# Optimization experiments

Measured on AMD Instinct MI355X. Metric: run time of the kernel, lower is better.

Reference implementation:

```python
import jax, jax.numpy as jnp
import numpy as np

N = 50000      # nodes
E = 400000     # edges (before self loops)
IN = 256       # in_channels
HID = 128      # hidden_channels
HEADS = 4
OUT = 256      # out_channels
NEG = 0.2      # LeakyReLU negative slope (PyG default)


def _glorot(key, shape, fan_in):
    return jax.random.normal(key, shape, jnp.float32) * (1.0 / np.sqrt(fan_in))


def setup_inputs() -> dict:
    key = jax.random.key(0)
    ks = jax.random.split(key, 8)
    x = jax.random.normal(ks[0], (N, IN), jnp.float32)
    edge_index = jax.random.randint(ks[1], (2, E), 0, N, dtype=jnp.int64)
    # layer 1: GATv2Conv(IN -> HID, heads=HEADS, concat=True)
    W1l = _glorot(ks[2], (IN, HEADS * HID), IN)           # source transform
    W1r = _glorot(ks[3], (IN, HEADS * HID), IN)           # target transform
    a1 = _glorot(ks[4], (HEADS, HID), HID)                # attention vector per head
    b1 = jnp.zeros((HEADS * HID,), jnp.float32)
    # layer 2: GATv2Conv(HEADS*HID -> OUT, heads=1, concat=False)
    W2l = _glorot(ks[5], (HEADS * HID, OUT), HEADS * HID)
    W2r = _glorot(ks[6], (HEADS * HID, OUT), HEADS * HID)
    a2 = _glorot(ks[7], (1, OUT), OUT)
    b2 = jnp.zeros((OUT,), jnp.float32)
    return dict(x=x, edge_index=edge_index, W1l=W1l, W1r=W1r, a1=a1, b1=b1,
                W2l=W2l, W2r=W2r, a2=a2, b2=b2)


def gatv2_conv(x, src, dst, Wl, Wr, att, bias, heads, ch, concat):
    """PyG GATv2Conv (add_self_loops already applied to src/dst).
    message j->i uses x_l[j]; score = att . leaky_relu(x_l[j] + x_r[i])."""
    n = x.shape[0]
    xl = (x @ Wl).reshape(n, heads, ch)   # [N,H,C] source features
    xr = (x @ Wr).reshape(n, heads, ch)   # [N,H,C] target features
    g = xl[src] + xr[dst]                 # [E',H,C] gathered per edge
    e = jnp.einsum('ehc,hc->eh', jax.nn.leaky_relu(g, NEG), att)  # [E',H]
    # segment softmax over incoming edges of each dst node
    e_max = jax.ops.segment_max(e, dst, num_segments=n)
    p = jnp.exp(e - e_max[dst])
    denom = jax.ops.segment_sum(p, dst, num_segments=n)
    alpha = p / denom[dst]                # [E',H]
    out = jax.ops.segment_sum(alpha[:, :, None] * xl[src], dst, num_segments=n)
    out = out.reshape(n, heads * ch) if concat else out.mean(axis=1)
    return out + bias


def reference(x, edge_index, W1l, W1r, a1, b1, W2l, W2r, a2, b2):
    loop = jnp.arange(x.shape[0], dtype=edge_index.dtype)
    src = jnp.concatenate([edge_index[0], loop])  # add self loops (PyG default)
    dst = jnp.concatenate([edge_index[1], loop])
    h = jax.nn.relu(gatv2_conv(x, src, dst, W1l, W1r, a1, b1, HEADS, HID, True))
    return gatv2_conv(h, src, dst, W2l, W2r, a2, b2, 1, OUT, False)
```

## Files before the change

kernel.cpp:

```cpp
#include <hip/hip_runtime.h>
#include <cstdint>
#include <cstddef>

#define NNODES 50000
#define NEDGES 400000
#define INC    256
#define D1     512
#define OUTC   256
#define NEG    0.2f
#define NB     196

typedef __attribute__((ext_vector_type(8))) short short8;
typedef __attribute__((ext_vector_type(4))) short bf16x4;
typedef __attribute__((ext_vector_type(4))) float f32x4;

__device__ inline short f2bf(float f) {
  union { float f; uint32_t u; } v; v.f = f;
  uint32_t r = (v.u + 0x7fffu + ((v.u >> 16) & 1u)) >> 16;
  return (short)(r & 0xffffu);
}
__device__ inline float bf2f(short s) {
  union { uint32_t u; float f; } v;
  v.u = ((uint32_t)(uint16_t)s) << 16;
  return v.f;
}

__global__ __launch_bounds__(256) void cvt_x_k(const float* __restrict__ x,
                                               short* __restrict__ xb) {
  size_t base = ((size_t)blockIdx.x * 256 + threadIdx.x) * 8;
  f32x4 a = *(const f32x4*)&x[base];
  f32x4 b = *(const f32x4*)&x[base + 4];
  short8 o;
  o[0] = f2bf(a[0]); o[1] = f2bf(a[1]); o[2] = f2bf(a[2]); o[3] = f2bf(a[3]);
  o[4] = f2bf(b[0]); o[5] = f2bf(b[1]); o[6] = f2bf(b[2]); o[7] = f2bf(b[3]);
  *(short8*)&xb[base] = o;
}

__global__ __launch_bounds__(256) void twb_k(const float* __restrict__ W,
                                             short* __restrict__ WT,
                                             int K, int N) {
  __shared__ float tile[32][33];
  int tx = threadIdx.x & 31, ty = threadIdx.x >> 5;
  int n0 = blockIdx.x * 32, k0 = blockIdx.y * 32;
#pragma unroll
  for (int i = 0; i < 4; ++i)
    tile[ty + i * 8][tx] = W[(size_t)(k0 + ty + i * 8) * N + n0 + tx];
  __syncthreads();
#pragma unroll
  for (int i = 0; i < 4; ++i) {
    int n = ty + i * 8;
    WT[(size_t)(n0 + n) * K + k0 + tx] = f2bf(tile[tx][n]);
  }
}

#define LDT 72
template<bool BF16OUT>
__global__ __launch_bounds__(256) void gemm_bf16_k(const short* __restrict__ A,
    const short* __restrict__ BT, void* __restrict__ Cv, int M, int K, int Nc) {
  __shared__ short As[128 * LDT];
  __shared__ short Bs[128 * LDT];
  const int tid = threadIdx.x;
  const int lane = tid & 63, wave = tid >> 6;
  const int wr = wave >> 1, wc = wave & 1;
  const int l15 = lane & 15, l4 = lane >> 4;
  const int bm = blockIdx.y * 128, bn = blockIdx.x * 128;

  f32x4 zero4 = {0.f, 0.f, 0.f, 0.f};
  f32x4 acc[4][4];
#pragma unroll
  for (int m = 0; m < 4; ++m)
#pragma unroll
    for (int n = 0; n < 4; ++n) acc[m][n] = zero4;

  for (int k0 = 0; k0 < K; k0 += 64) {
#pragma unroll
    for (int i = 0; i < 4; ++i) {
      int q = tid + 256 * i;
      int row = q >> 3, kc = q & 7;
      short8 va = {0, 0, 0, 0, 0, 0, 0, 0};
      int gr = bm + row;
      if (gr < M) va = *(const short8*)&A[(size_t)gr * K + k0 + kc * 8];
      *(short8*)&As[row * LDT + kc * 8] = va;
      short8 vb = *(const short8*)&BT[(size_t)(bn + row) * K + k0 + kc * 8];
      *(short8*)&Bs[row * LDT + kc * 8] = vb;
    }
    __syncthreads();
    short8 af[4][2], bf[4][2];
#pragma unroll
    for (int m = 0; m < 4; ++m)
#pragma unroll
      for (int kk = 0; kk < 2; ++kk)
        af[m][kk] = *(const short8*)&As[(wr * 64 + m * 16 + l15) * LDT + kk * 32 + l4 * 8];
#pragma unroll
    for (int n = 0; n < 4; ++n)
#pragma unroll
      for (int kk = 0; kk < 2; ++kk)
        bf[n][kk] = *(const short8*)&Bs[(wc * 64 + n * 16 + l15) * LDT + kk * 32 + l4 * 8];
#pragma unroll
    for (int kk = 0; kk < 2; ++kk)
#pragma unroll
      for (int m = 0; m < 4; ++m)
#pragma unroll
        for (int n = 0; n < 4; ++n)
          acc[m][n] = __builtin_amdgcn_mfma_f32_16x16x32_bf16(
              af[m][kk], bf[n][kk], acc[m][n], 0, 0, 0);
    __syncthreads();
  }
#pragma unroll
  for (int m = 0; m < 4; ++m) {
    int row0 = bm + wr * 64 + m * 16 + l4 * 4;
#pragma unroll
    for (int r = 0; r < 4; ++r) {
      int row = row0 + r;
      if (row < M) {
#pragma unroll
        for (int n = 0; n < 4; ++n) {
          size_t idx = (size_t)row * Nc + bn + wc * 64 + n * 16 + l15;
          if (BF16OUT) ((short*)Cv)[idx] = f2bf(acc[m][n][r]);
          else         ((float*)Cv)[idx] = acc[m][n][r];
        }
      }
    }
  }
}

__global__ __launch_bounds__(256) void zero_i_k(int* __restrict__ p, int n) {
  int stride = gridDim.x * 256;
  for (int i = blockIdx.x * 256 + threadIdx.x; i < n; i += stride) p[i] = 0;
}

__global__ __launch_bounds__(256) void hist_k(const int* __restrict__ dsts,
                                              int* __restrict__ deg) {
  int e = blockIdx.x * 256 + threadIdx.x;
  if (e < NEDGES) atomicAdd(&deg[dsts[e]], 1);
}

__global__ __launch_bounds__(256) void bsum_k(const int* __restrict__ deg,
                                              int* __restrict__ bsum) {
  __shared__ int red[256];
  int t = threadIdx.x, i = blockIdx.x * 256 + t;
  red[t] = (i < NNODES) ? deg[i] : 0;
  __syncthreads();
#pragma unroll
  for (int off = 128; off > 0; off >>= 1) {
    if (t < off) red[t] += red[t + off];
    __syncthreads();
  }
  if (t == 0) bsum[blockIdx.x] = red[0];
}

__global__ __launch_bounds__(64) void bscan_k(const int* __restrict__ bsum,
                                              int* __restrict__ bscan) {
  if (threadIdx.x == 0) {
    int run = 0;
    for (int j = 0; j < NB; ++j) { bscan[j] = run; run += bsum[j]; }
  }
}

__global__ __launch_bounds__(256) void rowptr_k(const int* __restrict__ deg,
    const int* __restrict__ bscan, int* __restrict__ rowptr,
    int* __restrict__ cursor) {
  __shared__ int s[256];
  int t = threadIdx.x, b = blockIdx.x, i = b * 256 + t;
  int v = (i < NNODES) ? deg[i] : 0;
  s[t] = v;
  __syncthreads();
#pragma unroll
  for (int off = 1; off < 256; off <<= 1) {
    int y = (t >= off) ? s[t - off] : 0;
    __syncthreads();
    s[t] += y;
    __syncthreads();
  }
  if (i < NNODES) {
    int ex = bscan[b] + s[t] - v;
    rowptr[i] = ex;
    cursor[i] = ex;
  }
  if (b == 0 && t == 0) rowptr[NNODES] = NEDGES;
}

__global__ __launch_bounds__(256) void scatter_k(const int* __restrict__ srcs,
    const int* __restrict__ dsts, int* __restrict__ cursor,
    int* __restrict__ col) {
  int e = blockIdx.x * 256 + threadIdx.x;
  if (e < NEDGES) {
    int pos = atomicAdd(&cursor[dsts[e]], 1);
    col[pos] = srcs[e];
  }
}

__global__ __launch_bounds__(256) void fused1_k(const int* __restrict__ rowptr,
    const int* __restrict__ col, const short* __restrict__ XLb,
    const float* __restrict__ XR, const float* __restrict__ a1,
    const float* __restrict__ b1, short* __restrict__ Hb) {
  int d = blockIdx.x * 4 + (threadIdx.x >> 6);
  if (d >= NNODES) return;
  int lane = threadIdx.x & 63;
  int c0 = lane * 8;
  float av[8], xr[8], acc[8];
#pragma unroll
  for (int t = 0; t < 8; ++t) {
    av[t] = a1[c0 + t];
    xr[t] = XR[(size_t)d * D1 + c0 + t];
    acc[t] = 0.f;
  }
  float den = 0.f;
  int beg = rowptr[d], end = rowptr[d + 1];
  for (int i = beg - 1; i < end; ++i) {
    int s = (i < beg) ? d : col[i];
    short8 v = *(const short8*)&XLb[(size_t)s * D1 + c0];
    float xl[8];
#pragma unroll
    for (int t = 0; t < 8; ++t) xl[t] = bf2f(v[t]);
    float part = 0.f;
#pragma unroll
    for (int t = 0; t < 8; ++t) {
      float g = xl[t] + xr[t];
      g = g > 0.f ? g : NEG * g;
      part = fmaf(g, av[t], part);
    }
    part += __shfl_xor(part, 1);
    part += __shfl_xor(part, 2);
    part += __shfl_xor(part, 4);
    part += __shfl_xor(part, 8);
    float p = __expf(part);
    den += p;
#pragma unroll
    for (int t = 0; t < 8; ++t) acc[t] = fmaf(p, xl[t], acc[t]);
  }
  short8 o;
#pragma unroll
  for (int t = 0; t < 8; ++t) {
    float hv = acc[t] / den + b1[c0 + t];
    hv = hv > 0.f ? hv : 0.f;
    o[t] = f2bf(hv);
  }
  *(short8*)&Hb[(size_t)d * D1 + c0] = o;
}

__global__ __launch_bounds__(256) void fused2_k(const int* __restrict__ rowptr,
    const int* __restrict__ col, const short* __restrict__ XLb,
    const float* __restrict__ XR, const float* __restrict__ a2,
    const float* __restrict__ b2, float* __restrict__ out) {
  int d = blockIdx.x * 4 + (threadIdx.x >> 6);
  if (d >= NNODES) return;
  int lane = threadIdx.x & 63;
  int c0 = lane * 4;
  float av[4], xr[4], acc[4];
#pragma unroll
  for (int t = 0; t < 4; ++t) {
    av[t] = a2[c0 + t];
    xr[t] = XR[(size_t)d * OUTC + c0 + t];
    acc[t] = 0.f;
  }
  float den = 0.f;
  int beg = rowptr[d], end = rowptr[d + 1];
  for (int i = beg - 1; i < end; ++i) {
    int s = (i < beg) ? d : col[i];
    bf16x4 v = *(const bf16x4*)&XLb[(size_t)s * OUTC + c0];
    float xl[4];
#pragma unroll
    for (int t = 0; t < 4; ++t) xl[t] = bf2f(v[t]);
    float part = 0.f;
#pragma unroll
    for (int t = 0; t < 4; ++t) {
      float g = xl[t] + xr[t];
      g = g > 0.f ? g : NEG * g;
      part = fmaf(g, av[t], part);
    }
#pragma unroll
    for (int off = 1; off < 64; off <<= 1) part += __shfl_xor(part, off);
    float p = __expf(part);
    den += p;
#pragma unroll
    for (int t = 0; t < 4; ++t) acc[t] = fmaf(p, xl[t], acc[t]);
  }
  f32x4 o;
#pragma unroll
  for (int t = 0; t < 4; ++t) o[t] = acc[t] / den + b2[c0 + t];
  *(f32x4*)&out[(size_t)d * OUTC + c0] = o;
}

extern "C" void kernel_launch(void* const* d_in, const int* in_sizes, int n_in,
                              void* d_out, int out_size, void* d_ws, size_t ws_size,
                              hipStream_t stream) {
  const float* x   = (const float*)d_in[0];
  const int*   ei  = (const int*)d_in[1];
  const float* W1l = (const float*)d_in[2];
  const float* W1r = (const float*)d_in[3];
  const float* a1  = (const float*)d_in[4];
  const float* b1  = (const float*)d_in[5];
  const float* W2l = (const float*)d_in[6];
  const float* W2r = (const float*)d_in[7];
  const float* a2  = (const float*)d_in[8];
  const float* b2  = (const float*)d_in[9];
  float* out = (float*)d_out;
  char* ws = (char*)d_ws;

  short* XL1b  = (short*)(ws + 0);
  float* XR1   = (float*)(ws + 51200000);
  short* XL2b  = (short*)(ws + 0);
  float* XR2   = (float*)(ws + 25600000);
  short* WT1l  = (short*)(ws + 153600000);
  short* WT1r  = (short*)(ws + 153862144);
  short* WT2l  = (short*)(ws + 154124288);
  short* WT2r  = (short*)(ws + 154386432);
  int* rowptr  = (int*)(ws + 154648576);
  int* cursor  = (int*)(ws + 154848640);
  int* colv    = (int*)(ws + 155048640);
  int* deg     = (int*)(ws + 156648640);
  int* bsum    = (int*)(ws + 156848640);
  int* bscan   = (int*)(ws + 156849536);
  short* XB = (short*)d_out;
  short* Hb = (short*)d_out;

  const int* srcs = ei;
  const int* dsts = ei + NEDGES;

  dim3 blk(256);
  int eblk = (NEDGES + 255) / 256;
  int nblk4 = (NNODES + 3) / 4;

  zero_i_k<<<64, blk, 0, stream>>>(deg, NNODES);
  hist_k<<<eblk, blk, 0, stream>>>(dsts, deg);
  bsum_k<<<NB, blk, 0, stream>>>(deg, bsum);
  bscan_k<<<1, 64, 0, stream>>>(bsum, bscan);
  rowptr_k<<<NB, blk, 0, stream>>>(deg, bscan, rowptr, cursor);
  scatter_k<<<eblk, blk, 0, stream>>>(srcs, dsts, cursor, colv);

  cvt_x_k<<<(NNODES * INC) / 2048, blk, 0, stream>>>(x, XB);
  twb_k<<<dim3(D1 / 32, INC / 32), blk, 0, stream>>>(W1l, WT1l, INC, D1);
  twb_k<<<dim3(D1 / 32, INC / 32), blk, 0, stream>>>(W1r, WT1r, INC, D1);
  twb_k<<<dim3(OUTC / 32, D1 / 32), blk, 0, stream>>>(W2l, WT2l, D1, OUTC);
  twb_k<<<dim3(OUTC / 32, D1 / 32), blk, 0, stream>>>(W2r, WT2r, D1, OUTC);

  dim3 g1(D1 / 128, (NNODES + 127) / 128);
  gemm_bf16_k<true ><<<g1, blk, 0, stream>>>(XB, WT1l, XL1b, NNODES, INC, D1);
  gemm_bf16_k<false><<<g1, blk, 0, stream>>>(XB, WT1r, XR1, NNODES, INC, D1);

  fused1_k<<<nblk4, blk, 0, stream>>>(rowptr, colv, XL1b, XR1, a1, b1, Hb);

  dim3 g2(OUTC / 128, (NNODES + 127) / 128);
  gemm_bf16_k<true ><<<g2, blk, 0, stream>>>(Hb, WT2l, XL2b, NNODES, D1, OUTC);
  gemm_bf16_k<false><<<g2, blk, 0, stream>>>(Hb, WT2r, XR2, NNODES, D1, OUTC);

  fused2_k<<<nblk4, blk, 0, stream>>>(rowptr, colv, XL2b, XR2, a2, b2, out);
}
```

Before: 494.4 us.

## Fuse left/right projections into one bf16 GEMM and unroll edge loop by two

The separate Wl and Wr weight transposes are concatenated so each layer runs a single GEMM producing an interleaved [N, 2*D] bf16 buffer. This replaces the fp32 XR output with bf16, halving that write and the later read. The aggregation kernels read xl and xr from the shared row, handle the self loop outside the main loop, and process two edges per iteration to overlap gathers and shuffle reductions. The change also stores xr at lower precision, which adds some rounding error, and widens the gathered row stride.

```diff
diff --git a/kernel.cpp b/kernel.cpp
--- a/kernel.cpp
+++ b/kernel.cpp
@@ -54,9 +54,8 @@
 }
 
 #define LDT 72
-template<bool BF16OUT>
 __global__ __launch_bounds__(256) void gemm_bf16_k(const short* __restrict__ A,
-    const short* __restrict__ BT, void* __restrict__ Cv, int M, int K, int Nc) {
+    const short* __restrict__ BT, short* __restrict__ C, int M, int K, int Nc) {
   __shared__ short As[128 * LDT];
   __shared__ short Bs[128 * LDT];
   const int tid = threadIdx.x;
@@ -114,11 +113,8 @@
       int row = row0 + r;
       if (row < M) {
 #pragma unroll
-        for (int n = 0; n < 4; ++n) {
-          size_t idx = (size_t)row * Nc + bn + wc * 64 + n * 16 + l15;
-          if (BF16OUT) ((short*)Cv)[idx] = f2bf(acc[m][n][r]);
-          else         ((float*)Cv)[idx] = acc[m][n][r];
-        }
+        for (int n = 0; n < 4; ++n)
+          C[(size_t)row * Nc + bn + wc * 64 + n * 16 + l15] = f2bf(acc[m][n][r]);
       }
     }
   }
@@ -191,82 +187,164 @@
 }
 
 __global__ __launch_bounds__(256) void fused1_k(const int* __restrict__ rowptr,
-    const int* __restrict__ col, const short* __restrict__ XLb,
-    const float* __restrict__ XR, const float* __restrict__ a1,
-    const float* __restrict__ b1, short* __restrict__ Hb) {
+    const int* __restrict__ col, const short* __restrict__ X1b,
+    const float* __restrict__ a1, const float* __restrict__ b1,
+    short* __restrict__ Hb) {
   int d = blockIdx.x * 4 + (threadIdx.x >> 6);
   if (d >= NNODES) return;
   int lane = threadIdx.x & 63;
   int c0 = lane * 8;
+  const size_t drow = (size_t)d * 1024;
   float av[8], xr[8], acc[8];
+  short8 vself = *(const short8*)&X1b[drow + c0];
+  short8 vxr   = *(const short8*)&X1b[drow + 512 + c0];
 #pragma unroll
   for (int t = 0; t < 8; ++t) {
     av[t] = a1[c0 + t];
-    xr[t] = XR[(size_t)d * D1 + c0 + t];
+    xr[t] = bf2f(vxr[t]);
     acc[t] = 0.f;
   }
   float den = 0.f;
-  int beg = rowptr[d], end = rowptr[d + 1];
-  for (int i = beg - 1; i < end; ++i) {
-    int s = (i < beg) ? d : col[i];
-    short8 v = *(const short8*)&XLb[(size_t)s * D1 + c0];
-    float xl[8];
-#pragma unroll
-    for (int t = 0; t < 8; ++t) xl[t] = bf2f(v[t]);
-    float part = 0.f;
+  {
+    float xl[8], part = 0.f;
 #pragma unroll
     for (int t = 0; t < 8; ++t) {
+      xl[t] = bf2f(vself[t]);
       float g = xl[t] + xr[t];
-      g = g > 0.f ? g : NEG * g;
+      g = fmaxf(g, NEG * g);
       part = fmaf(g, av[t], part);
     }
-    part += __shfl_xor(part, 1);
-    part += __shfl_xor(part, 2);
-    part += __shfl_xor(part, 4);
-    part += __shfl_xor(part, 8);
+    part += __shfl_xor(part, 1); part += __shfl_xor(part, 2);
+    part += __shfl_xor(part, 4); part += __shfl_xor(part, 8);
     float p = __expf(part);
     den += p;
 #pragma unroll
     for (int t = 0; t < 8; ++t) acc[t] = fmaf(p, xl[t], acc[t]);
   }
+  int beg = rowptr[d], end = rowptr[d + 1];
+  int i = beg;
+  for (; i + 1 < end; i += 2) {
+    int s0 = col[i], s1 = col[i + 1];
+    short8 v0 = *(const short8*)&X1b[(size_t)s0 * 1024 + c0];
+    short8 v1 = *(const short8*)&X1b[(size_t)s1 * 1024 + c0];
+    float xl0[8], xl1[8], p0 = 0.f, p1 = 0.f;
+#pragma unroll
+    for (int t = 0; t < 8; ++t) {
+      xl0[t] = bf2f(v0[t]);
+      float g0 = xl0[t] + xr[t]; g0 = fmaxf(g0, NEG * g0); p0 = fmaf(g0, av[t], p0);
+      xl1[t] = bf2f(v1[t]);
+      float g1 = xl1[t] + xr[t]; g1 = fmaxf(g1, NEG * g1); p1 = fmaf(g1, av[t], p1);
+    }
+    p0 += __shfl_xor(p0, 1); p1 += __shfl_xor(p1, 1);
+    p0 += __shfl_xor(p0, 2); p1 += __shfl_xor(p1, 2);
+    p0 += __shfl_xor(p0, 4); p1 += __shfl_xor(p1, 4);
+    p0 += __shfl_xor(p0, 8); p1 += __shfl_xor(p1, 8);
+    float e0 = __expf(p0), e1 = __expf(p1);
+    den += e0 + e1;
+#pragma unroll
+    for (int t = 0; t < 8; ++t) {
+      acc[t] = fmaf(e0, xl0[t], acc[t]);
+      acc[t] = fmaf(e1, xl1[t], acc[t]);
+    }
+  }
+  if (i < end) {
+    int s = col[i];
+    short8 v = *(const short8*)&X1b[(size_t)s * 1024 + c0];
+    float xl[8], part = 0.f;
+#pragma unroll
+    for (int t = 0; t < 8; ++t) {
+      xl[t] = bf2f(v[t]);
+      float g = xl[t] + xr[t];
+      g = fmaxf(g, NEG * g);
+      part = fmaf(g, av[t], part);
+    }
+    part += __shfl_xor(part, 1); part += __shfl_xor(part, 2);
+    part += __shfl_xor(part, 4); part += __shfl_xor(part, 8);
+    float p = __expf(part);
+    den += p;
+#pragma unroll
+    for (int t = 0; t < 8; ++t) acc[t] = fmaf(p, xl[t], acc[t]);
+  }
   short8 o;
 #pragma unroll
   for (int t = 0; t < 8; ++t) {
     float hv = acc[t] / den + b1[c0 + t];
-    hv = hv > 0.f ? hv : 0.f;
-    o[t] = f2bf(hv);
+    o[t] = f2bf(fmaxf(hv, 0.f));
   }
   *(short8*)&Hb[(size_t)d * D1 + c0] = o;
 }
 
 __global__ __launch_bounds__(256) void fused2_k(const int* __restrict__ rowptr,
-    const int* __restrict__ col, const short* __restrict__ XLb,
-    const float* __restrict__ XR, const float* __restrict__ a2,
-    const float* __restrict__ b2, float* __restrict__ out) {
+    const int* __restrict__ col, const short* __restrict__ X2b,
+    const float* __restrict__ a2, const float* __restrict__ b2,
+    float* __restrict__ out) {
   int d = blockIdx.x * 4 + (threadIdx.x >> 6);
   if (d >= NNODES) return;
   int lane = threadIdx.x & 63;
   int c0 = lane * 4;
+  const size_t drow = (size_t)d * 512;
   float av[4], xr[4], acc[4];
+  bf16x4 vself = *(const bf16x4*)&X2b[drow + c0];
+  bf16x4 vxr   = *(const bf16x4*)&X2b[drow + 256 + c0];
 #pragma unroll
   for (int t = 0; t < 4; ++t) {
     av[t] = a2[c0 + t];
-    xr[t] = XR[(size_t)d * OUTC + c0 + t];
+    xr[t] = bf2f(vxr[t]);
     acc[t] = 0.f;
   }
   float den = 0.f;
+  {
+    float xl[4], part = 0.f;
+#pragma unroll
+    for (int t = 0; t < 4; ++t) {
+      xl[t] = bf2f(vself[t]);
+      float g = xl[t] + xr[t];
+      g = fmaxf(g, NEG * g);
+      part = fmaf(g, av[t], part);
+    }
+#pragma unroll
+    for (int off = 1; off < 64; off <<= 1) part += __shfl_xor(part, off);
+    float p = __expf(part);
+    den += p;
+#pragma unroll
+    for (int t = 0; t < 4; ++t) acc[t] = fmaf(p, xl[t], acc[t]);
+  }
   int beg = rowptr[d], end = rowptr[d + 1];
-  for (int i = beg - 1; i < end; ++i) {
-    int s = (i < beg) ? d : col[i];
-    bf16x4 v = *(const bf16x4*)&XLb[(size_t)s * OUTC + c0];
-    float xl[4];
-#pragma unroll
-    for (int t = 0; t < 4; ++t) xl[t] = bf2f(v[t]);
-    float part = 0.f;
+  int i = beg;
+  for (; i + 1 < end; i += 2) {
+    int s0 = col[i], s1 = col[i + 1];
+    bf16x4 v0 = *(const bf16x4*)&X2b[(size_t)s0 * 512 + c0];
+    bf16x4 v1 = *(const bf16x4*)&X2b[(size_t)s1 * 512 + c0];
+    float xl0[4], xl1[4], p0 = 0.f, p1 = 0.f;
 #pragma unroll
     for (int t = 0; t < 4; ++t) {
+      xl0[t] = bf2f(v0[t]);
+      float g0 = xl0[t] + xr[t]; g0 = fmaxf(g0, NEG * g0); p0 = fmaf(g0, av[t], p0);
+      xl1[t] = bf2f(v1[t]);
+      float g1 = xl1[t] + xr[t]; g1 = fmaxf(g1, NEG * g1); p1 = fmaf(g1, av[t], p1);
+    }
+#pragma unroll
+    for (int off = 1; off < 64; off <<= 1) {
+      p0 += __shfl_xor(p0, off);
+      p1 += __shfl_xor(p1, off);
+    }
+    float e0 = __expf(p0), e1 = __expf(p1);
+    den += e0 + e1;
+#pragma unroll
+    for (int t = 0; t < 4; ++t) {
+      acc[t] = fmaf(e0, xl0[t], acc[t]);
+      acc[t] = fmaf(e1, xl1[t], acc[t]);
+    }
+  }
+  if (i < end) {
+    int s = col[i];
+    bf16x4 v = *(const bf16x4*)&X2b[(size_t)s * 512 + c0];
+    float xl[4], part = 0.f;
+#pragma unroll
+    for (int t = 0; t < 4; ++t) {
+      xl[t] = bf2f(v[t]);
       float g = xl[t] + xr[t];
-      g = g > 0.f ? g : NEG * g;
+      g = fmaxf(g, NEG * g);
       part = fmaf(g, av[t], part);
     }
 #pragma unroll
@@ -298,20 +376,16 @@
   float* out = (float*)d_out;
   char* ws = (char*)d_ws;
 
-  short* XL1b  = (short*)(ws + 0);
-  float* XR1   = (float*)(ws + 51200000);
-  short* XL2b  = (short*)(ws + 0);
-  float* XR2   = (float*)(ws + 25600000);
-  short* WT1l  = (short*)(ws + 153600000);
-  short* WT1r  = (short*)(ws + 153862144);
-  short* WT2l  = (short*)(ws + 154124288);
-  short* WT2r  = (short*)(ws + 154386432);
-  int* rowptr  = (int*)(ws + 154648576);
-  int* cursor  = (int*)(ws + 154848640);
-  int* colv    = (int*)(ws + 155048640);
-  int* deg     = (int*)(ws + 156648640);
-  int* bsum    = (int*)(ws + 156848640);
-  int* bscan   = (int*)(ws + 156849536);
+  short* X1b   = (short*)(ws + 0);
+  short* X2b   = (short*)(ws + 0);
+  short* WT1   = (short*)(ws + 102400000);
+  short* WT2   = (short*)(ws + 102924288);
+  int* rowptr  = (int*)(ws + 103448576);
+  int* cursor  = (int*)(ws + 103648640);
+  int* colv    = (int*)(ws + 103848640);
+  int* deg     = (int*)(ws + 105448640);
+  int* bsum    = (int*)(ws + 105648640);
+  int* bscan   = (int*)(ws + 105649536);
   short* XB = (short*)d_out;
   short* Hb = (short*)d_out;
 
@@ -330,20 +404,18 @@
   scatter_k<<<eblk, blk, 0, stream>>>(srcs, dsts, cursor, colv);
 
   cvt_x_k<<<(NNODES * INC) / 2048, blk, 0, stream>>>(x, XB);
-  twb_k<<<dim3(D1 / 32, INC / 32), blk, 0, stream>>>(W1l, WT1l, INC, D1);
-  twb_k<<<dim3(D1 / 32, INC / 32), blk, 0, stream>>>(W1r, WT1r, INC, D1);
-  twb_k<<<dim3(OUTC / 32, D1 / 32), blk, 0, stream>>>(W2l, WT2l, D1, OUTC);
-  twb_k<<<dim3(OUTC / 32, D1 / 32), blk, 0, stream>>>(W2r, WT2r, D1, OUTC);
-
-  dim3 g1(D1 / 128, (NNODES + 127) / 128);
-  gemm_bf16_k<true ><<<g1, blk, 0, stream>>>(XB, WT1l, XL1b, NNODES, INC, D1);
-  gemm_bf16_k<false><<<g1, blk, 0, stream>>>(XB, WT1r, XR1, NNODES, INC, D1);
-
-  fused1_k<<<nblk4, blk, 0, stream>>>(rowptr, colv, XL1b, XR1, a1, b1, Hb);
-
-  dim3 g2(OUTC / 128, (NNODES + 127) / 128);
-  gemm_bf16_k<true ><<<g2, blk, 0, stream>>>(Hb, WT2l, XL2b, NNODES, D1, OUTC);
-  gemm_bf16_k<false><<<g2, blk, 0, stream>>>(Hb, WT2r, XR2, NNODES, D1, OUTC);
-
-  fused2_k<<<nblk4, blk, 0, stream>>>(rowptr, colv, XL2b, XR2, a2, b2, out);
-}
+  twb_k<<<dim3(D1 / 32, INC / 32), blk, 0, stream>>>(W1l, WT1, INC, D1);
+  twb_k<<<dim3(D1 / 32, INC / 32), blk, 0, stream>>>(W1r, WT1 + 512 * 256, INC, D1);
+  twb_k<<<dim3(OUTC / 32, D1 / 32), blk, 0, stream>>>(W2l, WT2, D1, OUTC);
+  twb_k<<<dim3(OUTC / 32, D1 / 32), blk, 0, stream>>>(W2r, WT2 + 256 * 512, D1, OUTC);
+
+  gemm_bf16_k<<<dim3(1024 / 128, (NNODES + 127) / 128), blk, 0, stream>>>(
+      XB, WT1, X1b, NNODES, INC, 1024);
+
+  fused1_k<<<nblk4, blk, 0, stream>>>(rowptr, colv, X1b, a1, b1, Hb);
+
+  gemm_bf16_k<<<dim3(512 / 128, (NNODES + 127) / 128), blk, 0, stream>>>(
+      Hb, WT2, X2b, NNODES, D1, 512);
+
+  fused2_k<<<nblk4, blk, 0, stream>>>(rowptr, colv, X2b, a2, b2, out);
+}
```

After: 420.5 us. 1.18x faster.
